# Kernel tuning notes

Measured on AMD Instinct MI355X. Metric: run time of the kernel, lower is better.

## Reference

```python
import jax, jax.numpy as jnp
import numpy as np

B, C, H, W = 1024, 10, 30, 30


def setup_inputs() -> dict:
    key = jax.random.key(0)
    k1, k2, k3 = jax.random.split(key, 3)
    pred = jax.random.normal(k1, (B, C, H, W), dtype=jnp.float32)
    target = jax.random.normal(k2, (B, C, H, W), dtype=jnp.float32)
    input_grid = jax.random.normal(k3, (B, C, H, W), dtype=jnp.float32)
    return {"pred": pred, "target": target, "input_grid": input_grid}


def reference(pred, target, input_grid):
    dt = pred.dtype
    n_colors = pred.shape[1]
    pred_idx = jnp.argmax(pred, axis=1)      # [B,H,W]
    tgt_idx = jnp.argmax(target, axis=1)     # [B,H,W]
    inp_idx = jnp.argmax(input_grid, axis=1)  # [B,H,W]

    logp = jax.nn.log_softmax(pred, axis=1)  # [B,C,H,W]
    ce = -jnp.take_along_axis(logp, tgt_idx[:, None], axis=1)[:, 0]  # [B,H,W]
    incorrect = (pred_idx != tgt_idx).astype(dt)
    ce_loss = jnp.mean(ce * (1.0 + 4.0 * incorrect))

    exact_matches = jnp.all(pred_idx == tgt_idx, axis=(1, 2)).astype(dt)  # [B]
    exact_bonus = -1.0 * jnp.mean(exact_matches)

    should_not_copy = jnp.any(tgt_idx != inp_idx, axis=(1, 2)).astype(dt)
    did_copy = jnp.all(pred_idx == inp_idx, axis=(1, 2)).astype(dt)
    copy_penalty = 5.0 * jnp.mean(should_not_copy * did_copy)

    changed_pixels = jnp.mean((pred_idx != inp_idx).astype(dt), axis=(1, 2))  # [B]
    target_changed = jnp.mean((tgt_idx != inp_idx).astype(dt), axis=(1, 2))
    transform_diff = jnp.mean((changed_pixels - target_changed) ** 2)

    # color-set penalty (GPU-native replacement of per-batch unique/CPU loop):
    # a color is "present" iff any pixel has that index; missing = in target set but not pred set
    colors = jnp.arange(n_colors)
    pred_present = jnp.any(pred_idx[..., None] == colors, axis=(1, 2))  # [B,C] bool
    tgt_present = jnp.any(tgt_idx[..., None] == colors, axis=(1, 2))    # [B,C] bool
    missing = jnp.sum(tgt_present & jnp.logical_not(pred_present)).astype(dt)
    color_penalty = 0.1 * missing

    total = ce_loss + exact_bonus + copy_penalty + transform_diff + color_penalty
    total = jnp.where(jnp.isnan(total), jnp.asarray(2.0, dt),
                      jnp.where(total > 100.0, jnp.asarray(10.0, dt), total))
    return (total, ce_loss, copy_penalty, -exact_bonus, jnp.sum(exact_matches), transform_diff)
```

## Files before the change

kernel.cpp:

```cpp
#include <hip/hip_runtime.h>
#include <math.h>

constexpr int BATCH = 1024;
constexpr int NC    = 10;
constexpr int HW    = 900;
constexpr int PAIRS = 225;

__global__ __launch_bounds__(256, 4) void loss_main(
    const float* __restrict__ pred, const float* __restrict__ target,
    const float* __restrict__ inp, float4* __restrict__ ws) {
  const int img  = blockIdx.x >> 1;
  const int part = blockIdx.x & 1;
  const int t    = threadIdx.x;

  float ce_sum = 0.f;
  unsigned combo = 0;
  int counts = 0;

  if (t < PAIRS) {
    const size_t base = (size_t)img * NC * HW + part * (HW / 2) + t * 2;

    float2 p2[NC], t2[NC], g2[NC];
#pragma unroll
    for (int c = 0; c < NC; ++c) p2[c] = *(const float2*)(pred + base + c * HW);
#pragma unroll
    for (int c = 0; c < NC; ++c) t2[c] = *(const float2*)(target + base + c * HW);
#pragma unroll
    for (int c = 0; c < NC; ++c) g2[c] = *(const float2*)(inp + base + c * HW);

#pragma unroll
    for (int j = 0; j < 2; ++j) {
      float p[NC], tv[NC], gv[NC];
#pragma unroll
      for (int c = 0; c < NC; ++c) {
        p[c]  = j ? p2[c].y : p2[c].x;
        tv[c] = j ? t2[c].y : t2[c].x;
        gv[c] = j ? g2[c].y : g2[c].x;
      }

      float pmax = p[0]; int pidx = 0;
#pragma unroll
      for (int c = 1; c < NC; ++c)
        if (p[c] > pmax) { pmax = p[c]; pidx = c; }

      float s = 0.f;
#pragma unroll
      for (int c = 0; c < NC; ++c) s += __expf(p[c] - pmax);
      const float lse = pmax + __logf(s);

      float tmax = tv[0]; int tidx = 0;
#pragma unroll
      for (int c = 1; c < NC; ++c)
        if (tv[c] > tmax) { tmax = tv[c]; tidx = c; }
      float gmax = gv[0]; int gidx = 0;
#pragma unroll
      for (int c = 1; c < NC; ++c)
        if (gv[c] > gmax) { gmax = gv[c]; gidx = c; }

      float ptv = p[0];
#pragma unroll
      for (int c = 1; c < NC; ++c)
        if (tidx == c) ptv = p[c];

      const float ce = lse - ptv;
      const float w  = (pidx != tidx) ? 5.0f : 1.0f;
      ce_sum += ce * w;
      combo  |= (1u << pidx) | (1u << (10 + tidx));
      if (pidx != tidx) combo |= 1u << 20;
      if (tidx != gidx) combo |= 1u << 21;
      if (pidx != gidx) combo |= 1u << 22;
      counts += ((pidx != gidx) ? 1 : 0) + ((tidx != gidx) ? (1 << 16) : 0);
    }
  }

#pragma unroll
  for (int off = 32; off >= 1; off >>= 1) {
    ce_sum += __shfl_down(ce_sum, off);
    combo  |= __shfl_down(combo, off);
    counts += __shfl_down(counts, off);
  }

  __shared__ float s_ce[4];
  __shared__ unsigned s_or[4];
  __shared__ int s_cnt[4];
  const int wave = t >> 6;
  if ((t & 63) == 0) { s_ce[wave] = ce_sum; s_or[wave] = combo; s_cnt[wave] = counts; }
  __syncthreads();
  if (t == 0) {
    float4 slot;
    slot.x = s_ce[0] + s_ce[1] + s_ce[2] + s_ce[3];
    slot.y = __uint_as_float(s_or[0] | s_or[1] | s_or[2] | s_or[3]);
    slot.z = __int_as_float(s_cnt[0] + s_cnt[1] + s_cnt[2] + s_cnt[3]);
    slot.w = 0.f;
    ws[blockIdx.x] = slot;
  }
}

__global__ __launch_bounds__(1024) void loss_final(
    const float4* __restrict__ ws, float* __restrict__ out) {
  const int b = threadIdx.x;

  float ce = 0.f; unsigned orv = 0; int cnt = 0;
#pragma unroll
  for (int k = 0; k < 2; ++k) {
    const float4 v = ws[b * 2 + k];
    ce  += v.x;
    orv |= __float_as_uint(v.y);
    cnt += __float_as_int(v.z);
  }
  const int changed  = cnt & 0xFFFF;
  const int tchanged = cnt >> 16;
  const float exact   = (orv & (1u << 20)) ? 0.f : 1.f;
  const float any_ti  = (orv & (1u << 21)) ? 1.f : 0.f;
  const float all_pi  = (orv & (1u << 22)) ? 0.f : 1.f;
  const unsigned pm = orv & 0x3FFu, tm = (orv >> 10) & 0x3FFu;
  const float d = (float)(changed - tchanged) * (1.0f / (float)HW);

  float r_ce = ce;
  float r_ex = exact;
  float r_cp = any_ti * all_pi;
  float r_td = d * d;
  float r_mi = (float)__popc(tm & ~pm);

#pragma unroll
  for (int off = 32; off >= 1; off >>= 1) {
    r_ce += __shfl_down(r_ce, off);
    r_ex += __shfl_down(r_ex, off);
    r_cp += __shfl_down(r_cp, off);
    r_td += __shfl_down(r_td, off);
    r_mi += __shfl_down(r_mi, off);
  }

  __shared__ float red[16][5];
  const int wave = b >> 6;
  if ((b & 63) == 0) {
    red[wave][0] = r_ce; red[wave][1] = r_ex; red[wave][2] = r_cp;
    red[wave][3] = r_td; red[wave][4] = r_mi;
  }
  __syncthreads();
  if (b == 0) {
    float a0 = 0, a1 = 0, a2 = 0, a3 = 0, a4 = 0;
#pragma unroll
    for (int w = 0; w < 16; ++w) {
      a0 += red[w][0]; a1 += red[w][1]; a2 += red[w][2];
      a3 += red[w][3]; a4 += red[w][4];
    }
    const float ce_loss    = a0 * (1.0f / ((float)BATCH * (float)HW));
    const float exact_sum  = a1;
    const float exact_frac = exact_sum * (1.0f / (float)BATCH);
    const float copy_pen   = 5.0f * a2 * (1.0f / (float)BATCH);
    const float tdiff      = a3 * (1.0f / (float)BATCH);
    const float color_pen  = 0.1f * a4;
    float total = ce_loss - exact_frac + copy_pen + tdiff + color_pen;
    if (isnan(total)) total = 2.0f;
    else if (total > 100.0f) total = 10.0f;
    out[0] = total;
    out[1] = ce_loss;
    out[2] = copy_pen;
    out[3] = exact_frac;
    out[4] = exact_sum;
    out[5] = tdiff;
  }
}

extern "C" void kernel_launch(void* const* d_in, const int* in_sizes, int n_in,
                              void* d_out, int out_size, void* d_ws, size_t ws_size,
                              hipStream_t stream) {
  const float* pred   = (const float*)d_in[0];
  const float* target = (const float*)d_in[1];
  const float* inp    = (const float*)d_in[2];
  float4* ws = (float4*)d_ws;
  loss_main<<<dim3(BATCH * 2), dim3(256), 0, stream>>>(pred, target, inp, ws);
  loss_final<<<dim3(1), dim3(1024), 0, stream>>>(ws, (float*)d_out);
}
```

Baseline: 130.6 us.

## Use one block per image with float4 loads and staged per-tensor processing

Each block now covers a whole image, and each thread handles four pixels using 128-bit loads instead of two pixels with 64-bit loads. The three input tensors are loaded and reduced one after another (target, then pred, then input), so only one set of ten float4 registers is live at a time. This halves the grid and the workspace slots and simplifies the final reduction. In exchange there are fewer blocks in flight and less memory-level parallelism per thread, since the loads of the three tensors are now sequential. A leftover dead array is also added.

```diff
diff --git a/kernel.cpp b/kernel.cpp
--- a/kernel.cpp
+++ b/kernel.cpp
@@ -4,72 +4,92 @@
 constexpr int BATCH = 1024;
 constexpr int NC    = 10;
 constexpr int HW    = 900;
-constexpr int PAIRS = 225;
+constexpr int QUADS = 225;
 
 __global__ __launch_bounds__(256, 4) void loss_main(
     const float* __restrict__ pred, const float* __restrict__ target,
     const float* __restrict__ inp, float4* __restrict__ ws) {
-  const int img  = blockIdx.x >> 1;
-  const int part = blockIdx.x & 1;
-  const int t    = threadIdx.x;
+  const int img = blockIdx.x;
+  const int t   = threadIdx.x;
 
   float ce_sum = 0.f;
   unsigned combo = 0;
   int counts = 0;
 
-  if (t < PAIRS) {
-    const size_t base = (size_t)img * NC * HW + part * (HW / 2) + t * 2;
+  if (t < QUADS) {
+    const size_t base = (size_t)img * NC * HW + (size_t)t * 4;
 
-    float2 p2[NC], t2[NC], g2[NC];
+    int tidx[4];
+    {
+      float4 q[NC];
 #pragma unroll
-    for (int c = 0; c < NC; ++c) p2[c] = *(const float2*)(pred + base + c * HW);
+      for (int c = 0; c < NC; ++c) q[c] = *(const float4*)(target + base + c * HW);
+      float tm[4] = {q[0].x, q[0].y, q[0].z, q[0].w};
+      tidx[0] = tidx[1] = tidx[2] = tidx[3] = 0;
 #pragma unroll
-    for (int c = 0; c < NC; ++c) t2[c] = *(const float2*)(target + base + c * HW);
+      for (int c = 1; c < NC; ++c) {
+        const float v[4] = {q[c].x, q[c].y, q[c].z, q[c].w};
 #pragma unroll
-    for (int c = 0; c < NC; ++c) g2[c] = *(const float2*)(inp + base + c * HW);
+        for (int j = 0; j < 4; ++j)
+          if (v[j] > tm[j]) { tm[j] = v[j]; tidx[j] = c; }
+      }
+    }
 
+    int pidx[4];
+    {
+      float4 q[NC];
 #pragma unroll
-    for (int j = 0; j < 2; ++j) {
-      float p[NC], tv[NC], gv[NC];
+      for (int c = 0; c < NC; ++c) q[c] = *(const float4*)(pred + base + c * HW);
+      float pm[4] = {q[0].x, q[0].y, q[0].z, q[0].w};
+      float ptv[4] = {q[0].x, q[0].y, q[0].z, q[0].w};
+      pidx[0] = pidx[1] = pidx[2] = pidx[3] = 0;
 #pragma unroll
-      for (int c = 0; c < NC; ++c) {
-        p[c]  = j ? p2[c].y : p2[c].x;
-        tv[c] = j ? t2[c].y : t2[c].x;
-        gv[c] = j ? g2[c].y : g2[c].x;
+      for (int c = 1; c < NC; ++c) {
+        const float v[4] = {q[c].x, q[c].y, q[c].z, q[c].w};
+#pragma unroll
+        for (int j = 0; j < 4; ++j) {
+          if (v[j] > pm[j]) { pm[j] = v[j]; pidx[j] = c; }
+          if (tidx[j] == c) ptv[j] = v[j];
+        }
       }
+#pragma unroll
+      for (int j = 0; j < 4; ++j) {
+        const float pv[NC] = {q[0].x == q[0].x ? 0.f : 0.f, 0, 0, 0, 0, 0, 0, 0, 0, 0};
+        (void)pv;
+        float s = 0.f;
+#pragma unroll
+        for (int c = 0; c < NC; ++c) {
+          const float v = (j == 0) ? q[c].x : (j == 1) ? q[c].y : (j == 2) ? q[c].z : q[c].w;
+          s += __expf(v - pm[j]);
+        }
+        const float lse = pm[j] + __logf(s);
+        const float ce  = lse - ptv[j];
+        const float w   = (pidx[j] != tidx[j]) ? 5.0f : 1.0f;
+        ce_sum += ce * w;
+        combo  |= (1u << pidx[j]) | (1u << (10 + tidx[j]));
+        if (pidx[j] != tidx[j]) combo |= 1u << 20;
+      }
+    }
 
-      float pmax = p[0]; int pidx = 0;
+    {
+      float4 q[NC];
 #pragma unroll
-      for (int c = 1; c < NC; ++c)
-        if (p[c] > pmax) { pmax = p[c]; pidx = c; }
-
-      float s = 0.f;
+      for (int c = 0; c < NC; ++c) q[c] = *(const float4*)(inp + base + c * HW);
+      float gm[4] = {q[0].x, q[0].y, q[0].z, q[0].w};
+      int gidx[4] = {0, 0, 0, 0};
 #pragma unroll
-      for (int c = 0; c < NC; ++c) s += __expf(p[c] - pmax);
-      const float lse = pmax + __logf(s);
-
-      float tmax = tv[0]; int tidx = 0;
+      for (int c = 1; c < NC; ++c) {
+        const float v[4] = {q[c].x, q[c].y, q[c].z, q[c].w};
 #pragma unroll
-      for (int c = 1; c < NC; ++c)
-        if (tv[c] > tmax) { tmax = tv[c]; tidx = c; }
-      float gmax = gv[0]; int gidx = 0;
+        for (int j = 0; j < 4; ++j)
+          if (v[j] > gm[j]) { gm[j] = v[j]; gidx[j] = c; }
+      }
 #pragma unroll
-      for (int c = 1; c < NC; ++c)
-        if (gv[c] > gmax) { gmax = gv[c]; gidx = c; }
-
-      float ptv = p[0];
-#pragma unroll
-      for (int c = 1; c < NC; ++c)
-        if (tidx == c) ptv = p[c];
-
-      const float ce = lse - ptv;
-      const float w  = (pidx != tidx) ? 5.0f : 1.0f;
-      ce_sum += ce * w;
-      combo  |= (1u << pidx) | (1u << (10 + tidx));
-      if (pidx != tidx) combo |= 1u << 20;
-      if (tidx != gidx) combo |= 1u << 21;
-      if (pidx != gidx) combo |= 1u << 22;
-      counts += ((pidx != gidx) ? 1 : 0) + ((tidx != gidx) ? (1 << 16) : 0);
+      for (int j = 0; j < 4; ++j) {
+        if (tidx[j] != gidx[j]) combo |= 1u << 21;
+        if (pidx[j] != gidx[j]) combo |= 1u << 22;
+        counts += ((pidx[j] != gidx[j]) ? 1 : 0) + ((tidx[j] != gidx[j]) ? (1 << 16) : 0);
+      }
     }
   }
 
@@ -92,7 +112,7 @@
     slot.y = __uint_as_float(s_or[0] | s_or[1] | s_or[2] | s_or[3]);
     slot.z = __int_as_float(s_cnt[0] + s_cnt[1] + s_cnt[2] + s_cnt[3]);
     slot.w = 0.f;
-    ws[blockIdx.x] = slot;
+    ws[img] = slot;
   }
 }
 
@@ -100,19 +120,16 @@
     const float4* __restrict__ ws, float* __restrict__ out) {
   const int b = threadIdx.x;
 
-  float ce = 0.f; unsigned orv = 0; int cnt = 0;
-#pragma unroll
-  for (int k = 0; k < 2; ++k) {
-    const float4 v = ws[b * 2 + k];
-    ce  += v.x;
-    orv |= __float_as_uint(v.y);
-    cnt += __float_as_int(v.z);
-  }
+  const float4 v = ws[b];
+  const float ce = v.x;
+  const unsigned orv = __float_as_uint(v.y);
+  const int cnt = __float_as_int(v.z);
+
   const int changed  = cnt & 0xFFFF;
   const int tchanged = cnt >> 16;
-  const float exact   = (orv & (1u << 20)) ? 0.f : 1.f;
-  const float any_ti  = (orv & (1u << 21)) ? 1.f : 0.f;
-  const float all_pi  = (orv & (1u << 22)) ? 0.f : 1.f;
+  const float exact  = (orv & (1u << 20)) ? 0.f : 1.f;
+  const float any_ti = (orv & (1u << 21)) ? 1.f : 0.f;
+  const float all_pi = (orv & (1u << 22)) ? 0.f : 1.f;
   const unsigned pm = orv & 0x3FFu, tm = (orv >> 10) & 0x3FFu;
   const float d = (float)(changed - tchanged) * (1.0f / (float)HW);
 
@@ -170,6 +187,6 @@
   const float* target = (const float*)d_in[1];
   const float* inp    = (const float*)d_in[2];
   float4* ws = (float4*)d_ws;
-  loss_main<<<dim3(BATCH * 2), dim3(256), 0, stream>>>(pred, target, inp, ws);
+  loss_main<<<dim3(BATCH), dim3(256), 0, stream>>>(pred, target, inp, ws);
   loss_final<<<dim3(1), dim3(1024), 0, stream>>>(ws, (float*)d_out);
 }
```

New measurement: 133.6 us. +2.3%, slower.
